# Kernel optimization log

Measured on AMD Instinct MI355X. Metric: run time of the kernel, lower is better.

## Reference

```python
import jax, jax.numpy as jnp
import numpy as np

B, F, S, P, E, H = 64, 32, 512, 96, 8, 2048
TOP_K = 2
ALPHA = 10.0
ENT_EPS = 1e-8
CV_EPS = 1e-10


def setup_inputs() -> dict:
    key = jax.random.key(0)
    ks = jax.random.split(key, 8)
    s = 0.02
    return {
        "x": jax.random.normal(ks[0], (B, F, S), dtype=jnp.float32),
        "time_embedding": jax.random.normal(ks[1], (B, F, S), dtype=jnp.float32),
        "Wg": jax.random.normal(ks[2], (S, E), dtype=jnp.float32) * s,
        "bg": jnp.zeros((E,), dtype=jnp.float32),
        "W1": jax.random.normal(ks[3], (E, S, H), dtype=jnp.float32) * s,
        "b1": jnp.zeros((E, H), dtype=jnp.float32),
        "W2": jax.random.normal(ks[4], (E, H, P), dtype=jnp.float32) * s,
        "b2": jnp.zeros((E, P), dtype=jnp.float32),
    }


def _gates(tf, Wg, bg):
    # tf: [F, B, S] -> logits [F, B, E]
    logits = jnp.einsum('fbs,se->fbe', tf, Wg) + bg
    # kthvalue(x, E - top_k + 1) = (E - top_k)-th entry (0-based) of ascending sort = k-th largest
    kth = jnp.sort(logits, axis=-1)[..., E - TOP_K]  # [F, B]
    mask = logits < kth[..., None]
    sm = jax.nn.softmax(logits, axis=-1)
    dec = jnp.where(mask, ALPHA * jnp.log(sm + 1.0), ALPHA * (jnp.exp(sm) - 1.0))
    return jax.nn.softmax(dec, axis=-1)  # [F, B, E]


def reference(x, time_embedding, Wg, bg, W1, b1, W2, b2):
    xf = jnp.transpose(x, (1, 0, 2))               # [F, B, S]
    tf = jnp.transpose(time_embedding, (1, 0, 2))  # [F, B, S]
    gates = _gates(tf, Wg, bg)                     # [F, B, E]

    # all experts on all features (eval mode: dropout = identity)
    h = jax.nn.gelu(jnp.einsum('fbs,esh->febh', xf, W1) + b1[None, :, None, :], approximate=False)
    eo = jnp.einsum('febh,ehp->febp', h, W2) + b2[None, :, None, :]  # [F, E, B, P]
    out = jnp.einsum('fbe,febp->fbp', gates, eo)   # gated weighted sum
    output = jnp.transpose(out, (1, 0, 2))         # [B, F, P]

    # selector loss: cv_squared of importance = gates.sum(batch) expanded over pred_len
    gsum = gates.sum(axis=1)                       # [F, E]
    imp = jnp.broadcast_to(gsum[..., None], (F, E, P)).reshape(F, E * P)
    cv = jnp.var(imp, axis=1, ddof=1) / (jnp.mean(imp, axis=1) ** 2 + CV_EPS)
    selector_loss = jnp.sum(cv)                    # loss_coef = 1.0

    # entropy loss: importance1 = gates.mean(batch) expanded over pred_len
    gmean = gates.mean(axis=1)                     # [F, E]
    imp1 = jnp.broadcast_to(gmean[..., None], (F, E, P))
    entropy_loss = jnp.sum((-imp1 * jnp.log(imp1 + ENT_EPS)).mean(axis=(1, 2)))

    return output, selector_loss, entropy_loss
```

## Files before the change

kernel.cpp:

```cpp
#include <hip/hip_runtime.h>
#include <math.h>

#define B_ 64
#define F_ 32
#define S_ 512
#define P_ 96
#define E_ 8
#define H_ 2048
#define M_ 2048

#define BM 128
#define BH 128
#define BK 64
#define ZSPLIT 2
#define HPZ (H_ / ZSPLIT)
#define NHT (HPZ / BH)
#define NKC (S_ / BK)
#define HPITCH 136

typedef __bf16 bf16x8 __attribute__((ext_vector_type(8)));
typedef __bf16 bf16x4 __attribute__((ext_vector_type(4)));
typedef float f32x4 __attribute__((ext_vector_type(4)));

#define MFMA16(a, b, c) __builtin_amdgcn_mfma_f32_16x16x32_bf16((a), (b), (c), 0, 0, 0)

#define GLL16(gp, lp) __builtin_amdgcn_global_load_lds(                     \
    (const __attribute__((address_space(1))) void*)(gp),                    \
    (__attribute__((address_space(3))) void*)(lp), 16, 0, 0)

__device__ __forceinline__ float fast_gelu(float x) {
  float e = __builtin_amdgcn_exp2f(-2.45546696f * x);
  return x * __builtin_amdgcn_rcpf(1.0f + e);
}

#define PREP_GRID 3776

__global__ __launch_bounds__(256) void k_prep(const float* __restrict__ x,
                                              const float* __restrict__ te,
                                              const float* __restrict__ Wg,
                                              const float* __restrict__ bg,
                                              const float* __restrict__ W1,
                                              const float* __restrict__ W2,
                                              __bf16* __restrict__ xbf,
                                              __bf16* __restrict__ w1t,
                                              __bf16* __restrict__ w2t,
                                              float* __restrict__ gates,
                                              float* __restrict__ out) {
  __shared__ float tile[64 * 65];
  const int blk = blockIdx.x;
  const int tid = threadIdx.x;

  if (blk < 2048) {
    int e = blk >> 8, tt = blk & 255;
    int si = tt >> 5, hi = tt & 31;
    const float* src = W1 + (size_t)e * S_ * H_ + (size_t)(si * 64) * H_ + hi * 64;
    {
      int row = tid >> 2;
      int cb = (tid & 3) * 16;
#pragma unroll
      for (int k = 0; k < 4; ++k) {
        f32x4 v = *(const f32x4*)(src + (size_t)row * H_ + cb + k * 4);
#pragma unroll
        for (int u = 0; u < 4; ++u) tile[row * 65 + cb + k * 4 + u] = v[u];
      }
    }
    __syncthreads();
    {
      int h = tid >> 2;
      int sb = (tid & 3) * 16;
      __bf16* dst = w1t + (size_t)e * H_ * S_ + (size_t)(hi * 64 + h) * S_ + si * 64 + sb;
      bf16x8 o0, o1;
#pragma unroll
      for (int k = 0; k < 8; ++k) o0[k] = (__bf16)tile[(sb + k) * 65 + h];
#pragma unroll
      for (int k = 0; k < 8; ++k) o1[k] = (__bf16)tile[(sb + 8 + k) * 65 + h];
      *(bf16x8*)dst = o0;
      *(bf16x8*)(dst + 8) = o1;
    }
    return;
  }
  if (blk < 2560) {
    int t = blk - 2048;
    int e = t >> 6, hi = (t >> 1) & 31, ph = t & 1;
    const float* src = W2 + (size_t)e * H_ * P_ + (size_t)(hi * 64) * P_ + ph * 48;
    {
      int h = tid & 63;
      int seg = tid >> 6;
#pragma unroll
      for (int k = 0; k < 3; ++k) {
        f32x4 v = *(const f32x4*)(src + (size_t)h * P_ + seg * 12 + k * 4);
#pragma unroll
        for (int u = 0; u < 4; ++u) tile[h * 49 + seg * 12 + k * 4 + u] = v[u];
      }
    }
    __syncthreads();
    if (tid < 192) {
      int p = tid >> 2;
      int hb = (tid & 3) * 16;
      __bf16* dst = w2t + (size_t)e * P_ * H_ + (size_t)(ph * 48 + p) * H_ + hi * 64 + hb;
      bf16x8 o0, o1;
#pragma unroll
      for (int k = 0; k < 8; ++k) o0[k] = (__bf16)tile[(hb + k) * 49 + p];
#pragma unroll
      for (int k = 0; k < 8; ++k) o1[k] = (__bf16)tile[(hb + 8 + k) * 49 + p];
      *(bf16x8*)dst = o0;
      *(bf16x8*)(dst + 8) = o1;
    }
    return;
  }
  if (blk < 3072) {
    size_t i = (size_t)(blk - 2560) * 2048 + (size_t)tid * 8;
#pragma unroll
    for (int k = 0; k < 2; ++k) {
      f32x4 v = *(const f32x4*)(x + i + k * 4);
      bf16x4 o = {(__bf16)v[0], (__bf16)v[1], (__bf16)v[2], (__bf16)v[3]};
      *(bf16x4*)(xbf + i + k * 4) = o;
    }
    return;
  }
  if (blk < 3584) {
    int wave = tid >> 6, lane = tid & 63;
    int m = (blk - 3072) * 4 + wave;
    const float* trow = te + (size_t)m * S_;
    float acc[E_];
#pragma unroll
    for (int e = 0; e < E_; ++e) acc[e] = 0.f;
    for (int s = lane; s < S_; s += 64) {
      float t = trow[s];
      const f32x4* wgr = (const f32x4*)(Wg + s * E_);
      f32x4 a = wgr[0], b = wgr[1];
      acc[0] += t * a[0]; acc[1] += t * a[1]; acc[2] += t * a[2]; acc[3] += t * a[3];
      acc[4] += t * b[0]; acc[5] += t * b[1]; acc[6] += t * b[2]; acc[7] += t * b[3];
    }
#pragma unroll
    for (int e = 0; e < E_; ++e) {
#pragma unroll
      for (int off = 32; off > 0; off >>= 1) acc[e] += __shfl_xor(acc[e], off, 64);
    }
    if (lane == 0) {
      float lg[E_];
      float m1 = -3.4e38f, m2 = -3.4e38f;
#pragma unroll
      for (int e = 0; e < E_; ++e) {
        float v = acc[e] + bg[e];
        lg[e] = v;
        if (v > m1) { m2 = m1; m1 = v; }
        else if (v > m2) { m2 = v; }
      }
      float den = 0.f, sm[E_];
#pragma unroll
      for (int e = 0; e < E_; ++e) { sm[e] = expf(lg[e] - m1); den += sm[e]; }
      float inv = 1.f / den;
      float dmax = -3.4e38f, dec[E_];
#pragma unroll
      for (int e = 0; e < E_; ++e) {
        float p = sm[e] * inv;
        float d = (lg[e] < m2) ? (10.f * logf(p + 1.f)) : (10.f * (expf(p) - 1.f));
        dec[e] = d;
        dmax = fmaxf(dmax, d);
      }
      float dden = 0.f;
#pragma unroll
      for (int e = 0; e < E_; ++e) { dec[e] = expf(dec[e] - dmax); dden += dec[e]; }
      float dinv = 1.f / dden;
#pragma unroll
      for (int e = 0; e < E_; ++e) gates[m * E_ + e] = dec[e] * dinv;
    }
    return;
  }
  {
    size_t i = (size_t)(blk - 3584) * 1024 + (size_t)tid * 4;
    f32x4 z4 = {0.f, 0.f, 0.f, 0.f};
    *(f32x4*)(out + i) = z4;
  }
}

__global__ __launch_bounds__(512, 2) void k_experts(
    const __bf16* __restrict__ xbf,
    const __bf16* __restrict__ w1t,
    const __bf16* __restrict__ w2t,
    const float* __restrict__ b1,
    const float* __restrict__ b2,
    const float* __restrict__ gates,
    float* __restrict__ out)
{
  __shared__ __align__(16) __bf16 W1s[2][BH * BK];
  __shared__ __align__(16) __bf16 Xs[2][BM * BK];
  __shared__ __align__(16) __bf16 W2s[P_ * BH];
  __shared__ __align__(16) __bf16 Hs[BM * HPITCH];

  const int tid = threadIdx.x;

  if (blockIdx.z == ZSPLIT) {
    if (blockIdx.x != 0 || blockIdx.y != 0) return;
    float* gsum = (float*)&Hs[0];
    float* cvs  = gsum + F_ * E_;
    float* ents = cvs + F_;
    if (tid < 256) {
      int f = tid >> 3, ee = tid & 7;
      float s = 0.f;
      for (int b = 0; b < B_; ++b) s += gates[(size_t)(b * F_ + f) * E_ + ee];
      gsum[f * E_ + ee] = s;
    }
    __syncthreads();
    if (tid < F_) {
      float mean = 0.f;
#pragma unroll
      for (int k = 0; k < E_; ++k) mean += gsum[tid * E_ + k];
      mean *= (1.f / E_);
      float ss = 0.f;
#pragma unroll
      for (int k = 0; k < E_; ++k) { float d = gsum[tid * E_ + k] - mean; ss += d * d; }
      float var = (float)P_ * ss / (float)(E_ * P_ - 1);
      cvs[tid] = var / (mean * mean + 1e-10f);
      float ent = 0.f;
#pragma unroll
      for (int k = 0; k < E_; ++k) { float g = gsum[tid * E_ + k] * (1.f / B_); ent += -g * logf(g + 1e-8f); }
      ents[tid] = ent * (1.f / E_);
    }
    __syncthreads();
    if (tid == 0) {
      float a = 0.f, b = 0.f;
      for (int k = 0; k < F_; ++k) { a += cvs[k]; b += ents[k]; }
      out[(size_t)M_ * P_ + 0] = a;
      out[(size_t)M_ * P_ + 1] = b;
    }
    return;
  }

  const int wave = tid >> 6, lane = tid & 63;
  const int l15 = lane & 15, quad = lane >> 4;
  const int e = blockIdx.x;
  const int m0 = blockIdx.y * BM;
  const int hz = blockIdx.z * HPZ;

  const int sg = lane & 7;
  const int srl = lane >> 3;
  const int gcol = ((sg ^ srl) * 8);

  const __bf16* w1base = w1t + ((size_t)e * H_ + hz + wave * 16 + srl) * S_ + gcol;
  const __bf16* xg = xbf + (size_t)(m0 + wave * 16 + srl) * S_ + gcol;
  const __bf16* w2z = w2t + (size_t)e * P_ * H_ + hz;

  const int hq = (wave & 1) * 64;
  const int mq = (wave >> 1) * 32;
  const int w16 = wave * 16;

  const f32x4 fz = {0.f, 0.f, 0.f, 0.f};
  f32x4 acc1[4][2];
  f32x4 acc2[6];
#pragma unroll
  for (int j = 0; j < 6; ++j) acc2[j] = fz;

  auto STAGE = [&](int ht_, int kc_, int b) {
    const __bf16* w1p = w1base + (size_t)(ht_ * BH) * S_ + kc_ * BK;
    const __bf16* xp  = xg + kc_ * BK;
#pragma unroll
    for (int p = 0; p < 2; ++p) {
      GLL16(w1p + (size_t)(p * 8) * S_, &W1s[b][(wave * 16 + p * 8) * BK]);
      GLL16(xp  + (size_t)(p * 8) * S_, &Xs[b][(wave * 16 + p * 8) * BK]);
    }
  };

  auto STAGEW2 = [&](int ht_) {
#pragma unroll
    for (int p = 0; p < 3; ++p) {
      int r2 = wave * 12 + p * 4 + quad;
      GLL16(w2z + (size_t)r2 * H_ + ht_ * BH + ((l15 ^ (r2 & 7)) * 8),
            &W2s[(wave * 12 + p * 4) * BH]);
    }
  };

  auto COMPUTE = [&](int b) {
#pragma unroll
    for (int kk = 0; kk < 2; ++kk) {
      bf16x8 af[4], bx[2];
#pragma unroll
      for (int i = 0; i < 4; ++i) {
        int r = hq + i * 16 + l15;
        af[i] = *(const bf16x8*)&W1s[b][r * BK + (((kk * 4 + quad) ^ (r & 7)) * 8)];
      }
#pragma unroll
      for (int j = 0; j < 2; ++j) {
        int r = mq + j * 16 + l15;
        bx[j] = *(const bf16x8*)&Xs[b][r * BK + (((kk * 4 + quad) ^ (r & 7)) * 8)];
      }
#pragma unroll
      for (int i = 0; i < 4; ++i)
#pragma unroll
        for (int j = 0; j < 2; ++j)
          acc1[i][j] = MFMA16(af[i], bx[j], acc1[i][j]);
    }
  };

  auto GEMM2 = [&]() {
#pragma unroll
    for (int kk = 0; kk < 4; ++kk) {
      bf16x8 a = *(const bf16x8*)&Hs[(w16 + l15) * HPITCH + kk * 32 + quad * 8];
#pragma unroll
      for (int j = 0; j < 6; ++j) {
        bf16x8 bb = *(const bf16x8*)&W2s[(j * 16 + l15) * BH + (((kk * 4 + quad) ^ (l15 & 7)) * 8)];
        acc2[j] = MFMA16(a, bb, acc2[j]);
      }
    }
  };

  auto GELU = [&](int ht_) {
    const float* b1w = b1 + (size_t)e * H_ + hz + ht_ * BH + hq;
#pragma unroll
    for (int i = 0; i < 4; ++i) {
      f32x4 bv = *(const f32x4*)(b1w + i * 16 + quad * 4);
#pragma unroll
      for (int j = 0; j < 2; ++j) {
        bf16x4 hv;
#pragma unroll
        for (int r = 0; r < 4; ++r)
          hv[r] = (__bf16)fast_gelu(acc1[i][j][r] + bv[r]);
        *(bf16x4*)&Hs[(mq + j * 16 + l15) * HPITCH + hq + i * 16 + quad * 4] = hv;
      }
    }
  };

  STAGE(0, 0, 0);
  __syncthreads();

  for (int ht = 0; ht < NHT; ++ht) {
#pragma unroll
    for (int i = 0; i < 4; ++i)
#pragma unroll
      for (int j = 0; j < 2; ++j) acc1[i][j] = fz;

    int bsel = 0;
#pragma unroll
    for (int kc = 0; kc < NKC; ++kc) {
      if (kc < NKC - 1) {
        STAGE(ht, kc + 1, bsel ^ 1);
      } else {
        if (ht < NHT - 1) STAGE(ht + 1, 0, bsel ^ 1);
        STAGEW2(ht);
      }
      if (kc == 0 && ht > 0) GEMM2();
      COMPUTE(bsel);
      __syncthreads();
      bsel ^= 1;
    }
    GELU(ht);
    __syncthreads();
  }
  GEMM2();

#pragma unroll
  for (int r = 0; r < 4; ++r) {
    int m = m0 + w16 + quad * 4 + r;
    float g = gates[m * E_ + e];
#pragma unroll
    for (int j = 0; j < 6; ++j) {
      int col = j * 16 + l15;
      float v = acc2[j][r];
      if (blockIdx.z == 0) v += b2[e * P_ + col];
      atomicAdd(&out[(size_t)m * P_ + col], g * v);
    }
  }
}

extern "C" void kernel_launch(void* const* d_in, const int* in_sizes, int n_in,
                              void* d_out, int out_size, void* d_ws, size_t ws_size,
                              hipStream_t stream) {
  const float* x  = (const float*)d_in[0];
  const float* te = (const float*)d_in[1];
  const float* Wg = (const float*)d_in[2];
  const float* bg = (const float*)d_in[3];
  const float* W1 = (const float*)d_in[4];
  const float* b1 = (const float*)d_in[5];
  const float* W2 = (const float*)d_in[6];
  const float* b2 = (const float*)d_in[7];
  float* out = (float*)d_out;

  char* ws = (char*)d_ws;
  float* gates = (float*)ws;
  __bf16* xbf  = (__bf16*)(ws + 65536);
  __bf16* w1t  = (__bf16*)(ws + 65536 + 2097152);
  __bf16* w2t  = (__bf16*)(ws + 65536 + 2097152 + 16777216);

  k_prep<<<PREP_GRID, 256, 0, stream>>>(x, te, Wg, bg, W1, W2, xbf, w1t, w2t, gates, out);
  k_experts<<<dim3(E_, M_ / BM, ZSPLIT + 1), 512, 0, stream>>>(xbf, w1t, w2t, b1, b2, gates, out);
}
```

Measured before the change: 185.7 us.

## Deepen W1/X LDS pipeline, read W2 from global, swizzle H tile

Replaces the double-buffered W1/X staging with a 4-slot W1 ring and 3-slot X ring prefetched two and one chunks ahead. Hand-written s_waitcnt vmcnt plus s_barrier replace __syncthreads, so loads stay in flight across the barriers. W2 is now read directly from global memory in GEMM2 instead of being staged in LDS. The padded H tile becomes an XOR-swizzled unpadded layout, and s_setprio raises priority around the MFMA blocks. The risks are hand-counted vmcnt values that must match the outstanding loads exactly, and uncached global W2 reads that may add latency to GEMM2.

```diff
diff --git a/kernel.cpp b/kernel.cpp
--- a/kernel.cpp
+++ b/kernel.cpp
@@ -16,7 +16,6 @@
 #define HPZ (H_ / ZSPLIT)
 #define NHT (HPZ / BH)
 #define NKC (S_ / BK)
-#define HPITCH 136
 
 typedef __bf16 bf16x8 __attribute__((ext_vector_type(8)));
 typedef __bf16 bf16x4 __attribute__((ext_vector_type(4)));
@@ -27,6 +26,10 @@
 #define GLL16(gp, lp) __builtin_amdgcn_global_load_lds(                     \
     (const __attribute__((address_space(1))) void*)(gp),                    \
     (__attribute__((address_space(3))) void*)(lp), 16, 0, 0)
+
+#define PW4 asm volatile("s_waitcnt vmcnt(4) lgkmcnt(0)\n\ts_barrier" ::: "memory")
+#define PW2 asm volatile("s_waitcnt vmcnt(2) lgkmcnt(0)\n\ts_barrier" ::: "memory")
+#define PW0 asm volatile("s_waitcnt vmcnt(0) lgkmcnt(0)\n\ts_barrier" ::: "memory")
 
 __device__ __forceinline__ float fast_gelu(float x) {
   float e = __builtin_amdgcn_exp2f(-2.45546696f * x);
@@ -184,16 +187,15 @@
     const float* __restrict__ gates,
     float* __restrict__ out)
 {
-  __shared__ __align__(16) __bf16 W1s[2][BH * BK];
-  __shared__ __align__(16) __bf16 Xs[2][BM * BK];
-  __shared__ __align__(16) __bf16 W2s[P_ * BH];
-  __shared__ __align__(16) __bf16 Hs[BM * HPITCH];
+  __shared__ __align__(16) __bf16 W1s[4][BH * BK];
+  __shared__ __align__(16) __bf16 Xs[3][BM * BK];
+  __shared__ __align__(16) __bf16 Hs[BM * 128];
 
   const int tid = threadIdx.x;
 
   if (blockIdx.z == ZSPLIT) {
     if (blockIdx.x != 0 || blockIdx.y != 0) return;
-    float* gsum = (float*)&Hs[0];
+    float* gsum = (float*)&W1s[0][0];
     float* cvs  = gsum + F_ * E_;
     float* ents = cvs + F_;
     if (tid < 256) {
@@ -252,57 +254,55 @@
 #pragma unroll
   for (int j = 0; j < 6; ++j) acc2[j] = fz;
 
-  auto STAGE = [&](int ht_, int kc_, int b) {
-    const __bf16* w1p = w1base + (size_t)(ht_ * BH) * S_ + kc_ * BK;
-    const __bf16* xp  = xg + kc_ * BK;
-#pragma unroll
-    for (int p = 0; p < 2; ++p) {
-      GLL16(w1p + (size_t)(p * 8) * S_, &W1s[b][(wave * 16 + p * 8) * BK]);
-      GLL16(xp  + (size_t)(p * 8) * S_, &Xs[b][(wave * 16 + p * 8) * BK]);
-    }
-  };
-
-  auto STAGEW2 = [&](int ht_) {
-#pragma unroll
-    for (int p = 0; p < 3; ++p) {
-      int r2 = wave * 12 + p * 4 + quad;
-      GLL16(w2z + (size_t)r2 * H_ + ht_ * BH + ((l15 ^ (r2 & 7)) * 8),
-            &W2s[(wave * 12 + p * 4) * BH]);
-    }
-  };
-
-  auto COMPUTE = [&](int b) {
+  auto STAGE_W1 = [&](int slot, const __bf16* src) {
+#pragma unroll
+    for (int p = 0; p < 2; ++p)
+      GLL16(src + (size_t)(p * 8) * S_, &W1s[slot][(wave * 16 + p * 8) * BK]);
+  };
+  auto STAGE_X = [&](int slot, const __bf16* src) {
+#pragma unroll
+    for (int p = 0; p < 2; ++p)
+      GLL16(src + (size_t)(p * 8) * S_, &Xs[slot][(wave * 16 + p * 8) * BK]);
+  };
+
+  auto COMPUTE = [&](const __bf16* w1s, const __bf16* xs) {
 #pragma unroll
     for (int kk = 0; kk < 2; ++kk) {
       bf16x8 af[4], bx[2];
 #pragma unroll
       for (int i = 0; i < 4; ++i) {
         int r = hq + i * 16 + l15;
-        af[i] = *(const bf16x8*)&W1s[b][r * BK + (((kk * 4 + quad) ^ (r & 7)) * 8)];
+        af[i] = *(const bf16x8*)&w1s[r * BK + (((kk * 4 + quad) ^ (r & 7)) * 8)];
       }
 #pragma unroll
       for (int j = 0; j < 2; ++j) {
         int r = mq + j * 16 + l15;
-        bx[j] = *(const bf16x8*)&Xs[b][r * BK + (((kk * 4 + quad) ^ (r & 7)) * 8)];
-      }
+        bx[j] = *(const bf16x8*)&xs[r * BK + (((kk * 4 + quad) ^ (r & 7)) * 8)];
+      }
+      __builtin_amdgcn_s_setprio(1);
 #pragma unroll
       for (int i = 0; i < 4; ++i)
 #pragma unroll
         for (int j = 0; j < 2; ++j)
           acc1[i][j] = MFMA16(af[i], bx[j], acc1[i][j]);
-    }
-  };
-
-  auto GEMM2 = [&]() {
+      __builtin_amdgcn_s_setprio(0);
+    }
+  };
+
+  auto GEMM2 = [&](int htc) {
+    const __bf16* w2c = w2z + htc * BH;
+    __builtin_amdgcn_s_setprio(1);
 #pragma unroll
     for (int kk = 0; kk < 4; ++kk) {
-      bf16x8 a = *(const bf16x8*)&Hs[(w16 + l15) * HPITCH + kk * 32 + quad * 8];
+      int ab = (((w16 + l15) * 256) + (kk * 32 + quad * 8) * 2) ^ ((l15 & 7) << 4);
+      bf16x8 a = *(const bf16x8*)((const char*)Hs + ab);
 #pragma unroll
       for (int j = 0; j < 6; ++j) {
-        bf16x8 bb = *(const bf16x8*)&W2s[(j * 16 + l15) * BH + (((kk * 4 + quad) ^ (l15 & 7)) * 8)];
+        bf16x8 bb = *(const bf16x8*)(w2c + (size_t)(j * 16 + l15) * H_ + kk * 32 + quad * 8);
         acc2[j] = MFMA16(a, bb, acc2[j]);
       }
     }
+    __builtin_amdgcn_s_setprio(0);
   };
 
   auto GELU = [&](int ht_) {
@@ -316,38 +316,50 @@
 #pragma unroll
         for (int r = 0; r < 4; ++r)
           hv[r] = (__bf16)fast_gelu(acc1[i][j][r] + bv[r]);
-        *(bf16x4*)&Hs[(mq + j * 16 + l15) * HPITCH + hq + i * 16 + quad * 4] = hv;
-      }
-    }
-  };
-
-  STAGE(0, 0, 0);
-  __syncthreads();
-
+        int m = mq + j * 16 + l15;
+        int wb = (m * 256 + (hq + i * 16 + quad * 4) * 2) ^ ((l15 & 7) << 4);
+        *(bf16x4*)((char*)Hs + wb) = hv;
+      }
+    }
+  };
+
+  STAGE_W1(0, w1base);
+  STAGE_W1(1, w1base + BK);
+  STAGE_X(0, xg);
+
+  int xcur = 0;
   for (int ht = 0; ht < NHT; ++ht) {
 #pragma unroll
     for (int i = 0; i < 4; ++i)
 #pragma unroll
       for (int j = 0; j < 2; ++j) acc1[i][j] = fz;
 
-    int bsel = 0;
+    const __bf16* w1h = w1base + (size_t)(ht * BH) * S_;
+    const bool tail = (ht == NHT - 1);
+
 #pragma unroll
     for (int kc = 0; kc < NKC; ++kc) {
-      if (kc < NKC - 1) {
-        STAGE(ht, kc + 1, bsel ^ 1);
-      } else {
-        if (ht < NHT - 1) STAGE(ht + 1, 0, bsel ^ 1);
-        STAGEW2(ht);
-      }
-      if (kc == 0 && ht > 0) GEMM2();
-      COMPUTE(bsel);
-      __syncthreads();
-      bsel ^= 1;
+      if (kc <= 5) {
+        STAGE_W1((kc + 2) & 3, w1h + (kc + 2) * BK);
+      } else if (!tail) {
+        STAGE_W1((kc + 2) & 3, w1h + (size_t)BH * S_ + ((kc + 2) & 7) * BK);
+      }
+      int xnext = (xcur == 2) ? 0 : xcur + 1;
+      if (!(tail && kc == 7)) STAGE_X(xnext, xg + ((kc + 1) & 7) * BK);
+
+      if (!tail || kc <= 5)      { PW4; }
+      else if (kc == 6)          { PW2; }
+      else                       { PW0; }
+
+      if (kc == 0 && ht > 0) GEMM2(ht - 1);
+
+      COMPUTE(&W1s[kc & 3][0], &Xs[xcur][0]);
+      xcur = xnext;
     }
     GELU(ht);
-    __syncthreads();
-  }
-  GEMM2();
+  }
+  asm volatile("s_waitcnt lgkmcnt(0)\n\ts_barrier" ::: "memory");
+  GEMM2(NHT - 1);
 
 #pragma unroll
   for (int r = 0; r < 4; ++r) {
```

Measured after the change: 205.8 us. 1.11x slower.
